# Kernel optimization log

Measured on AMD Instinct MI355X. Metric: run time of the kernel, lower is better.

The kernel has to match this reference:

```python
import jax, jax.numpy as jnp
import numpy as np

NUM_NODES = 10000  # fixed by input spec: edge_index values in [0, 10000)


def setup_inputs() -> dict:
    key = jax.random.key(0)
    k1, k2, k3 = jax.random.split(key, 3)
    N, E, D_IN, D_OUT = NUM_NODES, 320000, 256, 256
    x = jax.random.normal(k1, (N, D_IN), dtype=jnp.float32)
    edge_index = jax.random.randint(k2, (2, E), 0, N, dtype=jnp.int64)
    # ensure node N-1 appears so num_nodes == N as in the torch code
    edge_index = edge_index.at[0, 0].set(N - 1)
    # xavier_uniform for [D_IN, D_OUT]
    limit = float(np.sqrt(6.0 / (D_IN + D_OUT)))
    weight = jax.random.uniform(k3, (D_IN, D_OUT), dtype=jnp.float32,
                                minval=-limit, maxval=limit)
    return {"x": x, "edge_index": edge_index, "weight": weight}


def _normalize_adjacency(edge_index, num_nodes):
    src, dst = edge_index[0], edge_index[1]
    ones = jnp.ones(src.shape[0], dtype=jnp.float32)
    # symmetric binarized adjacency: adj[i,j] = adj[j,i] = 1 (set, not add)
    adj = jnp.zeros((num_nodes, num_nodes), dtype=jnp.float32)
    adj = adj.at[src, dst].max(ones)
    adj = adj.at[dst, src].max(ones)
    # one round of self-loops: adj += I
    adj = adj + jnp.eye(num_nodes, dtype=jnp.float32)
    deg = jnp.sum(adj, axis=1)                    # [N]
    dinv = 1.0 / jnp.sqrt(deg)                    # [N]
    # D^-1/2 A D^-1/2 via broadcasting (equivalent to diag mms)
    return adj * dinv[:, None] * dinv[None, :]


def reference(x, edge_index, weight):
    adj = _normalize_adjacency(edge_index, NUM_NODES)  # [N, N]
    h = adj @ x                                        # [N, D_IN]
    return h @ weight                                  # [N, D_OUT]
```

## Files before the change

### kernel.cpp

```cpp
#include <hip/hip_runtime.h>
#include <hip/hip_bf16.h>
#include <stdint.h>

#define N_NODES   10000
#define D_FEAT    256
#define E_EDGES   320000
#define ROW_WORDS 313
#define ROW_STRIDE 320
#define LIST_CAP  1024

#define NB     250
#define RPB    40
#define B_CAP  8192
#define NBLK_E 313
#define NBLK_W 64
#define RPC    10
#define NBLK_C 1000
#define NBLK_G 625
#define COLSTR 128

#define LDSTR 264

typedef __attribute__((ext_vector_type(4))) float float4v;
typedef _Float16 half8  __attribute__((ext_vector_type(8)));
typedef _Float16 half4v __attribute__((ext_vector_type(4)));

__device__ __forceinline__ float h2f_lo(uint32_t u) {
    union { uint32_t u; _Float16 h[2]; } v; v.u = u; return (float)v.h[0];
}
__device__ __forceinline__ float h2f_hi(uint32_t u) {
    union { uint32_t u; _Float16 h[2]; } v; v.u = u; return (float)v.h[1];
}


__global__ void __launch_bounds__(1024)
fill_buckets(const int* __restrict__ ei, uint32_t* __restrict__ bucketbuf,
             uint32_t* __restrict__ cursors,
             const float* __restrict__ w, _Float16* __restrict__ wt) {
    __shared__ uint32_t hist[256];
    __shared__ uint32_t lofs[256];
    __shared__ uint32_t base_s[256];
    __shared__ uint32_t stage[2048];
    __shared__ uint16_t sbkt[2048];
    int t = threadIdx.x;

    if (blockIdx.x >= NBLK_E) {
        int kb = (blockIdx.x - NBLK_E) * 4;
        int k = kb + (t >> 8), n = t & 255;
        float* st = (float*)stage;
        st[(n << 2) | (t >> 8)] = w[(size_t)k * D_FEAT + n];
        __syncthreads();
        if (t < 256) {
            half4v o = { (_Float16)st[t * 4 + 0], (_Float16)st[t * 4 + 1],
                         (_Float16)st[t * 4 + 2], (_Float16)st[t * 4 + 3] };
            *(half4v*)&wt[(size_t)t * D_FEAT + kb] = o;
        }
        return;
    }

    if (t < 256) hist[t] = 0;
    __syncthreads();
    int e = blockIdx.x * 1024 + t;
    int b0 = -1, b1 = -1; uint32_t ent0 = 0, ent1 = 0, s0 = 0, s1 = 0;
    if (e < E_EDGES) {
        int s = ei[e], d = ei[E_EDGES + e];
        if ((uint32_t)s < N_NODES && (uint32_t)d < N_NODES) {
            b0 = s / RPB; ent0 = ((uint32_t)(s - b0 * RPB) << 14) | (uint32_t)d;
            b1 = d / RPB; ent1 = ((uint32_t)(d - b1 * RPB) << 14) | (uint32_t)s;
            s0 = atomicAdd(&hist[b0], 1u);
            s1 = atomicAdd(&hist[b1], 1u);
        }
    }
    __syncthreads();
    if (t < 256) lofs[t] = hist[t];
    __syncthreads();
    for (int d = 1; d < 256; d <<= 1) {
        uint32_t v = 0;
        if (t < 256 && t >= d) v = lofs[t - d];
        __syncthreads();
        if (t < 256) lofs[t] += v;
        __syncthreads();
    }
    if (t < 256) base_s[t] = hist[t] ? atomicAdd(&cursors[t], hist[t]) : 0u;
    if (b0 >= 0) {
        uint32_t p0 = lofs[b0] - hist[b0] + s0;
        stage[p0] = ent0; sbkt[p0] = (uint16_t)b0;
        uint32_t p1 = lofs[b1] - hist[b1] + s1;
        stage[p1] = ent1; sbkt[p1] = (uint16_t)b1;
    }
    __syncthreads();
    uint32_t total = lofs[255];
    for (uint32_t idx = t; idx < total; idx += 1024) {
        uint32_t b = sbkt[idx];
        uint32_t pos = base_s[b] + (idx - (lofs[b] - hist[b]));
        if (pos < B_CAP) bucketbuf[(size_t)b * B_CAP + pos] = stage[idx];
    }
}

__global__ void __launch_bounds__(1024)
csr_gemm(const uint32_t* __restrict__ bucketbuf, const uint32_t* __restrict__ cursors,
         uint32_t* __restrict__ row_deg, float* __restrict__ dinv,
         uint32_t* __restrict__ col,
         const float* __restrict__ x, const _Float16* __restrict__ wt,
         _Float16* __restrict__ yw) {
    __shared__ __align__(16) uint32_t smem[RPC * ROW_WORDS];
    int t = threadIdx.x;

    if (blockIdx.x >= NBLK_C) {
        _Float16* a_lds = (_Float16*)smem;
        int r0 = (blockIdx.x - NBLK_C) * 16;
        int row = t >> 6, c4 = (t & 63) * 4;
        float4v xv = *(const float4v*)(x + (size_t)(r0 + row) * D_FEAT + c4);
        half4v h = { (_Float16)xv[0], (_Float16)xv[1],
                     (_Float16)xv[2], (_Float16)xv[3] };
        *(half4v*)&a_lds[row * LDSTR + c4] = h;
        __syncthreads();
        int wv = t >> 6, lane = t & 63;
        int quad = lane >> 4, r = lane & 15;
        int ct = wv;
        const _Float16* pb = wt + (size_t)(ct * 16 + r) * D_FEAT + quad * 8;
        float4v acc = {0.f, 0.f, 0.f, 0.f};
        #pragma unroll
        for (int kk = 0; kk < D_FEAT; kk += 32) {
            half8 a = *(const half8*)&a_lds[r * LDSTR + kk + quad * 8];
            half8 b = *(const half8*)(pb + kk);
            acc = __builtin_amdgcn_mfma_f32_16x16x32_f16(a, b, acc, 0, 0, 0);
        }
        int colg = ct * 16 + r;
        #pragma unroll
        for (int u = 0; u < 4; u++)
            yw[(size_t)(r0 + quad * 4 + u) * D_FEAT + colg] = (_Float16)acc[u];
        return;
    }

    uint32_t* bm = smem;
    int b   = blockIdx.x >> 2;
    int lr0 = (blockIdx.x & 3) * RPC;
    for (int i = t; i < RPC * ROW_WORDS; i += 1024) bm[i] = 0;
    __syncthreads();
    uint32_t cnt = min(cursors[b], (uint32_t)B_CAP);
    const uint32_t* bb = bucketbuf + (size_t)b * B_CAP;
    for (uint32_t i = t; i < cnt; i += 1024) {
        uint32_t ent = bb[i];
        uint32_t lr = (ent >> 14) - (uint32_t)lr0;
        if (lr < RPC) {
            uint32_t d = ent & 0x3FFFu;
            atomicOr(&bm[lr * ROW_WORDS + (d >> 5)], 1u << (d & 31));
        }
    }
    __syncthreads();
    int wv = t >> 6, lane = t & 63;
    for (int r = wv; r < RPC; r += 16) {
        int gi = b * RPB + lr0 + r;
        uint32_t wb[5]; int tot = 0;
        #pragma unroll
        for (int k = 0; k < 5; k++) {
            int w = lane + 64 * k;
            uint32_t v = (w < ROW_WORDS) ? bm[r * ROW_WORDS + w] : 0u;
            wb[k] = v; tot += __popc(v);
        }
        int incl = tot;
        #pragma unroll
        for (int off = 1; off < 64; off <<= 1) {
            int v = __shfl_up(incl, off, 64);
            if (lane >= off) incl += v;
        }
        uint32_t total = (uint32_t)__shfl(incl, 63, 64);
        if (lane == 0) {
            row_deg[gi] = min(total, (uint32_t)COLSTR);
            dinv[gi]    = 1.0f / sqrtf((float)(total + 1u));
        }
        uint32_t p = (uint32_t)(incl - tot);
        #pragma unroll
        for (int k = 0; k < 5; k++) {
            uint32_t bits = wb[k];
            uint32_t cbase = (uint32_t)(lane + 64 * k) << 5;
            while (bits) {
                if (p < COLSTR)
                    col[(size_t)gi * COLSTR + p] = cbase + (uint32_t)__builtin_ctz(bits);
                p++;
                bits &= bits - 1;
            }
        }
    }
}

__global__ void __launch_bounds__(256)
spmm_out(const uint32_t* __restrict__ row_deg, const float* __restrict__ dinv,
         const uint32_t* __restrict__ col, const _Float16* __restrict__ ywp,
         float* __restrict__ out) {
    const uint16_t* yw = (const uint16_t*)ywp;
    int wv = threadIdx.x >> 6, lane = threadIdx.x & 63;
    int i = blockIdx.x * 4 + wv;
    uint32_t base = (uint32_t)i * COLSTR;
    uint32_t deg = min(row_deg[i], (uint32_t)COLSTR);
    float di = dinv[i];
    float4v z = {0.f, 0.f, 0.f, 0.f};
    float4v a0 = z, a1 = z, a2 = z, a3 = z, a4 = z, a5 = z, a6 = z, a7 = z;
    size_t ch = (size_t)lane * 4;
    uint32_t t8 = deg & ~7u;
    uint32_t t = 0;
    for (; t < t8; t += 8) {
        uint4 jva = *(const uint4*)&col[base + t];
        uint4 jvb = *(const uint4*)&col[base + t + 4];
        float d0 = dinv[jva.x], d1 = dinv[jva.y], d2 = dinv[jva.z], d3 = dinv[jva.w];
        float d4 = dinv[jvb.x], d5 = dinv[jvb.y], d6 = dinv[jvb.z], d7 = dinv[jvb.w];
        uint2 g0 = *(const uint2*)(yw + (size_t)jva.x * D_FEAT + ch);
        uint2 g1 = *(const uint2*)(yw + (size_t)jva.y * D_FEAT + ch);
        uint2 g2 = *(const uint2*)(yw + (size_t)jva.z * D_FEAT + ch);
        uint2 g3 = *(const uint2*)(yw + (size_t)jva.w * D_FEAT + ch);
        uint2 g4 = *(const uint2*)(yw + (size_t)jvb.x * D_FEAT + ch);
        uint2 g5 = *(const uint2*)(yw + (size_t)jvb.y * D_FEAT + ch);
        uint2 g6 = *(const uint2*)(yw + (size_t)jvb.z * D_FEAT + ch);
        uint2 g7 = *(const uint2*)(yw + (size_t)jvb.w * D_FEAT + ch);
        a0[0] += d0 * h2f_lo(g0.x); a0[1] += d0 * h2f_hi(g0.x);
        a0[2] += d0 * h2f_lo(g0.y); a0[3] += d0 * h2f_hi(g0.y);
        a1[0] += d1 * h2f_lo(g1.x); a1[1] += d1 * h2f_hi(g1.x);
        a1[2] += d1 * h2f_lo(g1.y); a1[3] += d1 * h2f_hi(g1.y);
        a2[0] += d2 * h2f_lo(g2.x); a2[1] += d2 * h2f_hi(g2.x);
        a2[2] += d2 * h2f_lo(g2.y); a2[3] += d2 * h2f_hi(g2.y);
        a3[0] += d3 * h2f_lo(g3.x); a3[1] += d3 * h2f_hi(g3.x);
        a3[2] += d3 * h2f_lo(g3.y); a3[3] += d3 * h2f_hi(g3.y);
        a4[0] += d4 * h2f_lo(g4.x); a4[1] += d4 * h2f_hi(g4.x);
        a4[2] += d4 * h2f_lo(g4.y); a4[3] += d4 * h2f_hi(g4.y);
        a5[0] += d5 * h2f_lo(g5.x); a5[1] += d5 * h2f_hi(g5.x);
        a5[2] += d5 * h2f_lo(g5.y); a5[3] += d5 * h2f_hi(g5.y);
        a6[0] += d6 * h2f_lo(g6.x); a6[1] += d6 * h2f_hi(g6.x);
        a6[2] += d6 * h2f_lo(g6.y); a6[3] += d6 * h2f_hi(g6.y);
        a7[0] += d7 * h2f_lo(g7.x); a7[1] += d7 * h2f_hi(g7.x);
        a7[2] += d7 * h2f_lo(g7.y); a7[3] += d7 * h2f_hi(g7.y);
    }
    for (; t < deg; t++) {
        uint32_t j = col[base + t];
        float dj = dinv[j];
        uint2 g = *(const uint2*)(yw + (size_t)j * D_FEAT + ch);
        a0[0] += dj * h2f_lo(g.x); a0[1] += dj * h2f_hi(g.x);
        a0[2] += dj * h2f_lo(g.y); a0[3] += dj * h2f_hi(g.y);
    }
    uint2 gs = *(const uint2*)(yw + (size_t)i * D_FEAT + ch);
    a1[0] += di * h2f_lo(gs.x); a1[1] += di * h2f_hi(gs.x);
    a1[2] += di * h2f_lo(gs.y); a1[3] += di * h2f_hi(gs.y);
    float4v acc = ((a0 + a1) + (a2 + a3)) + ((a4 + a5) + (a6 + a7));
    *(float4v*)(out + (size_t)i * D_FEAT + ch) = di * acc;
}


__global__ void scatter_edges_fb(const int* __restrict__ ei,
                                 uint32_t* __restrict__ bitmap) {
    int e = blockIdx.x * blockDim.x + threadIdx.x;
    if (e >= E_EDGES) return;
    int s = ei[e], d = ei[E_EDGES + e];
    if ((uint32_t)s >= N_NODES || (uint32_t)d >= N_NODES) return;
    atomicOr(&bitmap[(size_t)s * ROW_STRIDE + (d >> 5)], 1u << (d & 31));
    atomicOr(&bitmap[(size_t)d * ROW_STRIDE + (s >> 5)], 1u << (s & 31));
}

__global__ void __launch_bounds__(256)
popc_dinv(const uint32_t* __restrict__ bitmap, float* __restrict__ dinv) {
    int wv = threadIdx.x >> 6, lane = threadIdx.x & 63;
    int i = blockIdx.x * 4 + wv;
    const uint32_t* rb = bitmap + (size_t)i * ROW_STRIDE;
    int pop = 0;
    #pragma unroll
    for (int k = 0; k < 5; k++) {
        int w = lane + 64 * k;
        if (w < ROW_WORDS) pop += __popc(rb[w]);
    }
    #pragma unroll
    for (int off = 32; off > 0; off >>= 1) pop += __shfl_xor(pop, off, 64);
    if (lane == 0) dinv[i] = 1.0f / sqrtf((float)(pop + 1));
}

__global__ void __launch_bounds__(256)
spmm_bitmap_fb(const uint32_t* __restrict__ bitmap, const float* __restrict__ dinv,
               const float* __restrict__ xf, float* __restrict__ agg) {
    __shared__ __align__(16) uint32_t lists[4][LIST_CAP];
    int wv = threadIdx.x >> 6, lane = threadIdx.x & 63;
    int i = blockIdx.x * 4 + wv;
    uint32_t* list = lists[wv];
    const uint32_t* rb = bitmap + (size_t)i * ROW_STRIDE;

    uint32_t wbits[5]; int tot = 0;
    #pragma unroll
    for (int k = 0; k < 5; k++) {
        int w = lane + 64 * k;
        uint32_t b = (w < ROW_WORDS) ? rb[w] : 0u;
        wbits[k] = b;
        tot += __popc(b);
    }
    int incl = tot;
    #pragma unroll
    for (int off = 1; off < 64; off <<= 1) {
        int v = __shfl_up(incl, off, 64);
        if (lane >= off) incl += v;
    }
    uint32_t p = (uint32_t)(incl - tot);
    uint32_t deg = (uint32_t)__shfl(incl, 63, 64);
    #pragma unroll
    for (int k = 0; k < 5; k++) {
        uint32_t bits = wbits[k];
        uint32_t base = (uint32_t)(lane + 64 * k) << 5;
        while (bits) {
            if (p < LIST_CAP) list[p] = base + (uint32_t)__builtin_ctz(bits);
            p++;
            bits &= bits - 1;
        }
    }
    if (deg > LIST_CAP) deg = LIST_CAP;

    float di = dinv[i];
    float4v z = {0.f, 0.f, 0.f, 0.f};
    float4v acc0 = z, acc1 = z, acc2 = z, acc3 = z;
    float4v sv = *(const float4v*)(xf + (size_t)i * D_FEAT + lane * 4);
    uint32_t t4 = deg & ~3u;
    for (uint32_t k = 0; k < t4; k += 4) {
        uint4 jv = *(const uint4*)&list[k];
        float d0 = dinv[jv.x], d1 = dinv[jv.y], d2 = dinv[jv.z], d3 = dinv[jv.w];
        float4v v0 = *(const float4v*)(xf + (size_t)jv.x * D_FEAT + lane * 4);
        float4v v1 = *(const float4v*)(xf + (size_t)jv.y * D_FEAT + lane * 4);
        float4v v2 = *(const float4v*)(xf + (size_t)jv.z * D_FEAT + lane * 4);
        float4v v3 = *(const float4v*)(xf + (size_t)jv.w * D_FEAT + lane * 4);
        acc0 += d0 * v0; acc1 += d1 * v1; acc2 += d2 * v2; acc3 += d3 * v3;
    }
    for (uint32_t k = t4; k < deg; k++) {
        uint32_t j = list[k];
        acc0 += dinv[j] * (*(const float4v*)(xf + (size_t)j * D_FEAT + lane * 4));
    }
    float4v acc = (acc0 + acc1) + (acc2 + acc3) + di * sv;
    *(float4v*)(agg + (size_t)i * D_FEAT + lane * 4) = di * acc;
}

__global__ void __launch_bounds__(256)
gemm_valu(float* __restrict__ io, const float* __restrict__ wf) {
    __shared__ __align__(16) float a_lds[16 * D_FEAT];
    int c = threadIdx.x;
    int r0 = blockIdx.x * 16;
    for (int idx = c; idx < 16 * D_FEAT; idx += 256)
        a_lds[idx] = io[(size_t)r0 * D_FEAT + idx];
    __syncthreads();
    float acc[16];
    #pragma unroll
    for (int r = 0; r < 16; r++) acc[r] = 0.f;
    for (int k0 = 0; k0 < D_FEAT; k0 += 4) {
        float w0 = wf[(size_t)(k0 + 0) * D_FEAT + c];
        float w1 = wf[(size_t)(k0 + 1) * D_FEAT + c];
        float w2 = wf[(size_t)(k0 + 2) * D_FEAT + c];
        float w3 = wf[(size_t)(k0 + 3) * D_FEAT + c];
        #pragma unroll
        for (int r = 0; r < 16; r++) {
            float4v av = *(const float4v*)&a_lds[r * D_FEAT + k0];
            acc[r] = fmaf(av[3], w3, fmaf(av[2], w2,
                     fmaf(av[1], w1, fmaf(av[0], w0, acc[r]))));
        }
    }
    #pragma unroll
    for (int r = 0; r < 16; r++)
        io[(size_t)(r0 + r) * D_FEAT + c] = acc[r];
}

extern "C" void kernel_launch(void* const* d_in, const int* in_sizes, int n_in,
                              void* d_out, int out_size, void* d_ws, size_t ws_size,
                              hipStream_t stream) {
    const float* x  = (const float*)d_in[0];
    const int*   ei = (const int*)d_in[1];
    const float* w  = (const float*)d_in[2];
    float* out = (float*)d_out;
    uint8_t* ws = (uint8_t*)d_ws;

    const size_t BB_OFF   = 1024;
    const size_t RD_OFF   = 8193024;
    const size_t DI_OFF   = 8233024;
    const size_t WT_OFF   = 8273024;
    const size_t YW_OFF   = 8404096;
    const size_t COL_OFF  = 13524096;
    const size_t NEED_NEW = 18644096;
    const size_t NEED_FB  = 12840000;

    if (ws_size >= NEED_NEW) {
        uint32_t* cursors   = (uint32_t*)ws;
        uint32_t* bucketbuf = (uint32_t*)(ws + BB_OFF);
        uint32_t* row_deg   = (uint32_t*)(ws + RD_OFF);
        float*    dinv      = (float*)(ws + DI_OFF);
        _Float16* wt        = (_Float16*)(ws + WT_OFF);
        _Float16* yw        = (_Float16*)(ws + YW_OFF);
        uint32_t* col       = (uint32_t*)(ws + COL_OFF);

        hipMemsetAsync(cursors, 0, 1024, stream);
        fill_buckets<<<NBLK_E + NBLK_W, 1024, 0, stream>>>(ei, bucketbuf, cursors, w, wt);
        csr_gemm    <<<NBLK_C + NBLK_G, 1024, 0, stream>>>(bucketbuf, cursors,
                                                           row_deg, dinv, col, x, wt, yw);
        spmm_out    <<<N_NODES / 4, 256, 0, stream>>>(row_deg, dinv, col, yw, out);
    } else if (ws_size >= NEED_FB) {
        uint32_t* bitmap = (uint32_t*)ws;
        float*    dinv   = (float*)(ws + 12800000);

        hipMemsetAsync(bitmap, 0, 12800000, stream);
        scatter_edges_fb<<<(E_EDGES + 255) / 256, 256, 0, stream>>>(ei, bitmap);
        popc_dinv      <<<N_NODES / 4, 256, 0, stream>>>(bitmap, dinv);
        spmm_bitmap_fb <<<N_NODES / 4, 256, 0, stream>>>(bitmap, dinv, x, out);
        gemm_valu      <<<N_NODES / 16, 256, 0, stream>>>(out, w);
    }
}
```

Baseline: 136.5 us.

## Use 1000 fine buckets of 10 rows and 16-bit column indices

Edges are now bucketed into 1000 buckets of 10 rows each instead of 250 buckets of 40 rows. Each csr_gemm block owns a whole bucket, so it no longer scans four times as many entries and discards those outside its row range. Column indices are stored as uint16, which halves the index traffic in spmm_out. In exchange the bucketing kernel does a 1024-entry LDS scan and more global atomics on cursors. The bucket capacity of 1024 entries risks overflow: the expected load is about 640 per bucket, and entries past capacity are silently dropped.

```diff
diff --git a/kernel.cpp b/kernel.cpp
--- a/kernel.cpp
+++ b/kernel.cpp
@@ -9,12 +9,11 @@
 #define ROW_STRIDE 320
 #define LIST_CAP  1024
 
-#define NB     250
-#define RPB    40
-#define B_CAP  8192
+#define NB     1000
+#define RPB    10
+#define B_CAP  1024
 #define NBLK_E 313
 #define NBLK_W 64
-#define RPC    10
 #define NBLK_C 1000
 #define NBLK_G 625
 #define COLSTR 128
@@ -34,12 +33,12 @@
 
 
 __global__ void __launch_bounds__(1024)
-fill_buckets(const int* __restrict__ ei, uint32_t* __restrict__ bucketbuf,
-             uint32_t* __restrict__ cursors,
-             const float* __restrict__ w, _Float16* __restrict__ wt) {
-    __shared__ uint32_t hist[256];
-    __shared__ uint32_t lofs[256];
-    __shared__ uint32_t base_s[256];
+fill_sort(const int* __restrict__ ei, uint32_t* __restrict__ bucketbuf,
+          uint32_t* __restrict__ cursors,
+          const float* __restrict__ w, _Float16* __restrict__ wt) {
+    __shared__ uint32_t hist[1024];
+    __shared__ uint32_t lofs[1024];
+    __shared__ uint32_t base_s[1024];
     __shared__ uint32_t stage[2048];
     __shared__ uint16_t sbkt[2048];
     int t = threadIdx.x;
@@ -58,7 +57,7 @@
         return;
     }
 
-    if (t < 256) hist[t] = 0;
+    hist[t] = 0;
     __syncthreads();
     int e = blockIdx.x * 1024 + t;
     int b0 = -1, b1 = -1; uint32_t ent0 = 0, ent1 = 0, s0 = 0, s1 = 0;
@@ -72,16 +71,15 @@
         }
     }
     __syncthreads();
-    if (t < 256) lofs[t] = hist[t];
-    __syncthreads();
-    for (int d = 1; d < 256; d <<= 1) {
-        uint32_t v = 0;
-        if (t < 256 && t >= d) v = lofs[t - d];
+    lofs[t] = hist[t];
+    __syncthreads();
+    for (int d = 1; d < 1024; d <<= 1) {
+        uint32_t v = (t >= d) ? lofs[t - d] : 0;
         __syncthreads();
-        if (t < 256) lofs[t] += v;
+        lofs[t] += v;
         __syncthreads();
     }
-    if (t < 256) base_s[t] = hist[t] ? atomicAdd(&cursors[t], hist[t]) : 0u;
+    base_s[t] = hist[t] ? atomicAdd(&cursors[t], hist[t]) : 0u;
     if (b0 >= 0) {
         uint32_t p0 = lofs[b0] - hist[b0] + s0;
         stage[p0] = ent0; sbkt[p0] = (uint16_t)b0;
@@ -89,7 +87,7 @@
         stage[p1] = ent1; sbkt[p1] = (uint16_t)b1;
     }
     __syncthreads();
-    uint32_t total = lofs[255];
+    uint32_t total = lofs[1023];
     for (uint32_t idx = t; idx < total; idx += 1024) {
         uint32_t b = sbkt[idx];
         uint32_t pos = base_s[b] + (idx - (lofs[b] - hist[b]));
@@ -100,10 +98,10 @@
 __global__ void __launch_bounds__(1024)
 csr_gemm(const uint32_t* __restrict__ bucketbuf, const uint32_t* __restrict__ cursors,
          uint32_t* __restrict__ row_deg, float* __restrict__ dinv,
-         uint32_t* __restrict__ col,
+         uint16_t* __restrict__ col,
          const float* __restrict__ x, const _Float16* __restrict__ wt,
          _Float16* __restrict__ yw) {
-    __shared__ __align__(16) uint32_t smem[RPC * ROW_WORDS];
+    __shared__ __align__(16) uint32_t smem[RPB * ROW_WORDS];
     int t = threadIdx.x;
 
     if (blockIdx.x >= NBLK_C) {
@@ -134,24 +132,21 @@
     }
 
     uint32_t* bm = smem;
-    int b   = blockIdx.x >> 2;
-    int lr0 = (blockIdx.x & 3) * RPC;
-    for (int i = t; i < RPC * ROW_WORDS; i += 1024) bm[i] = 0;
+    int b = blockIdx.x;
+    for (int i = t; i < RPB * ROW_WORDS; i += 1024) bm[i] = 0;
     __syncthreads();
     uint32_t cnt = min(cursors[b], (uint32_t)B_CAP);
     const uint32_t* bb = bucketbuf + (size_t)b * B_CAP;
     for (uint32_t i = t; i < cnt; i += 1024) {
         uint32_t ent = bb[i];
-        uint32_t lr = (ent >> 14) - (uint32_t)lr0;
-        if (lr < RPC) {
-            uint32_t d = ent & 0x3FFFu;
-            atomicOr(&bm[lr * ROW_WORDS + (d >> 5)], 1u << (d & 31));
-        }
+        uint32_t lr = ent >> 14, d = ent & 0x3FFFu;
+        atomicOr(&bm[lr * ROW_WORDS + (d >> 5)], 1u << (d & 31));
     }
     __syncthreads();
     int wv = t >> 6, lane = t & 63;
-    for (int r = wv; r < RPC; r += 16) {
-        int gi = b * RPB + lr0 + r;
+    if (wv < RPB) {
+        int r = wv;
+        int gi = b * RPB + r;
         uint32_t wb[5]; int tot = 0;
         #pragma unroll
         for (int k = 0; k < 5; k++) {
@@ -177,7 +172,8 @@
             uint32_t cbase = (uint32_t)(lane + 64 * k) << 5;
             while (bits) {
                 if (p < COLSTR)
-                    col[(size_t)gi * COLSTR + p] = cbase + (uint32_t)__builtin_ctz(bits);
+                    col[(size_t)gi * COLSTR + p] =
+                        (uint16_t)(cbase + (uint32_t)__builtin_ctz(bits));
                 p++;
                 bits &= bits - 1;
             }
@@ -187,7 +183,7 @@
 
 __global__ void __launch_bounds__(256)
 spmm_out(const uint32_t* __restrict__ row_deg, const float* __restrict__ dinv,
-         const uint32_t* __restrict__ col, const _Float16* __restrict__ ywp,
+         const uint16_t* __restrict__ col, const _Float16* __restrict__ ywp,
          float* __restrict__ out) {
     const uint16_t* yw = (const uint16_t*)ywp;
     int wv = threadIdx.x >> 6, lane = threadIdx.x & 63;
@@ -201,18 +197,21 @@
     uint32_t t8 = deg & ~7u;
     uint32_t t = 0;
     for (; t < t8; t += 8) {
-        uint4 jva = *(const uint4*)&col[base + t];
-        uint4 jvb = *(const uint4*)&col[base + t + 4];
-        float d0 = dinv[jva.x], d1 = dinv[jva.y], d2 = dinv[jva.z], d3 = dinv[jva.w];
-        float d4 = dinv[jvb.x], d5 = dinv[jvb.y], d6 = dinv[jvb.z], d7 = dinv[jvb.w];
-        uint2 g0 = *(const uint2*)(yw + (size_t)jva.x * D_FEAT + ch);
-        uint2 g1 = *(const uint2*)(yw + (size_t)jva.y * D_FEAT + ch);
-        uint2 g2 = *(const uint2*)(yw + (size_t)jva.z * D_FEAT + ch);
-        uint2 g3 = *(const uint2*)(yw + (size_t)jva.w * D_FEAT + ch);
-        uint2 g4 = *(const uint2*)(yw + (size_t)jvb.x * D_FEAT + ch);
-        uint2 g5 = *(const uint2*)(yw + (size_t)jvb.y * D_FEAT + ch);
-        uint2 g6 = *(const uint2*)(yw + (size_t)jvb.z * D_FEAT + ch);
-        uint2 g7 = *(const uint2*)(yw + (size_t)jvb.w * D_FEAT + ch);
+        uint4 cv = *(const uint4*)&col[base + t];
+        uint32_t j0 = cv.x & 0xffffu, j1 = cv.x >> 16;
+        uint32_t j2 = cv.y & 0xffffu, j3 = cv.y >> 16;
+        uint32_t j4 = cv.z & 0xffffu, j5 = cv.z >> 16;
+        uint32_t j6 = cv.w & 0xffffu, j7 = cv.w >> 16;
+        float d0 = dinv[j0], d1 = dinv[j1], d2 = dinv[j2], d3 = dinv[j3];
+        float d4 = dinv[j4], d5 = dinv[j5], d6 = dinv[j6], d7 = dinv[j7];
+        uint2 g0 = *(const uint2*)(yw + (size_t)j0 * D_FEAT + ch);
+        uint2 g1 = *(const uint2*)(yw + (size_t)j1 * D_FEAT + ch);
+        uint2 g2 = *(const uint2*)(yw + (size_t)j2 * D_FEAT + ch);
+        uint2 g3 = *(const uint2*)(yw + (size_t)j3 * D_FEAT + ch);
+        uint2 g4 = *(const uint2*)(yw + (size_t)j4 * D_FEAT + ch);
+        uint2 g5 = *(const uint2*)(yw + (size_t)j5 * D_FEAT + ch);
+        uint2 g6 = *(const uint2*)(yw + (size_t)j6 * D_FEAT + ch);
+        uint2 g7 = *(const uint2*)(yw + (size_t)j7 * D_FEAT + ch);
         a0[0] += d0 * h2f_lo(g0.x); a0[1] += d0 * h2f_hi(g0.x);
         a0[2] += d0 * h2f_lo(g0.y); a0[3] += d0 * h2f_hi(g0.y);
         a1[0] += d1 * h2f_lo(g1.x); a1[1] += d1 * h2f_hi(g1.x);
@@ -367,13 +366,13 @@
     float* out = (float*)d_out;
     uint8_t* ws = (uint8_t*)d_ws;
 
-    const size_t BB_OFF   = 1024;
-    const size_t RD_OFF   = 8193024;
-    const size_t DI_OFF   = 8233024;
-    const size_t WT_OFF   = 8273024;
-    const size_t YW_OFF   = 8404096;
-    const size_t COL_OFF  = 13524096;
-    const size_t NEED_NEW = 18644096;
+    const size_t BB_OFF   = 4096;
+    const size_t RD_OFF   = 4100096;
+    const size_t DI_OFF   = 4140096;
+    const size_t WT_OFF   = 4180096;
+    const size_t YW_OFF   = 4311168;
+    const size_t COL_OFF  = 9431168;
+    const size_t NEED_NEW = 11991168;
     const size_t NEED_FB  = 12840000;
 
     if (ws_size >= NEED_NEW) {
@@ -383,13 +382,13 @@
         float*    dinv      = (float*)(ws + DI_OFF);
         _Float16* wt        = (_Float16*)(ws + WT_OFF);
         _Float16* yw        = (_Float16*)(ws + YW_OFF);
-        uint32_t* col       = (uint32_t*)(ws + COL_OFF);
-
-        hipMemsetAsync(cursors, 0, 1024, stream);
-        fill_buckets<<<NBLK_E + NBLK_W, 1024, 0, stream>>>(ei, bucketbuf, cursors, w, wt);
-        csr_gemm    <<<NBLK_C + NBLK_G, 1024, 0, stream>>>(bucketbuf, cursors,
-                                                           row_deg, dinv, col, x, wt, yw);
-        spmm_out    <<<N_NODES / 4, 256, 0, stream>>>(row_deg, dinv, col, yw, out);
+        uint16_t* col       = (uint16_t*)(ws + COL_OFF);
+
+        hipMemsetAsync(cursors, 0, 4096, stream);
+        fill_sort<<<NBLK_E + NBLK_W, 1024, 0, stream>>>(ei, bucketbuf, cursors, w, wt);
+        csr_gemm <<<NBLK_C + NBLK_G, 1024, 0, stream>>>(bucketbuf, cursors,
+                                                        row_deg, dinv, col, x, wt, yw);
+        spmm_out <<<N_NODES / 4, 256, 0, stream>>>(row_deg, dinv, col, yw, out);
     } else if (ws_size >= NEED_FB) {
         uint32_t* bitmap = (uint32_t*)ws;
         float*    dinv   = (float*)(ws + 12800000);
```

After: 132.1 us. 1.03x faster.
